# Optimization experiments

Hardware: AMD Instinct MI355X
Metric: run time of the kernel (lower is better)

## Reference

```python
import jax, jax.numpy as jnp
import numpy as np

D_MODEL = 192; D_STATE = 16; D_CONV = 4; D_INNER = 384; DT_RANK = 12; DEPTH = 8
B = 1; T = 8; IMG = 224; P = 16; GT = 8; GH = 14; GW = 14; L = 1 + GT * GH * GW
LN_EPS = 1e-5


def _layernorm(x, g, b):
    m = jnp.mean(x, -1, keepdims=True)
    v = jnp.var(x, -1, keepdims=True)
    return (x - m) * jax.lax.rsqrt(v + LN_EPS) * g + b


def _silu(x):
    return x * jax.nn.sigmoid(x)


def _mamba(h, W_in, Wc, bc, Wx, W_dt, b_dt, A_log, Dp, W_out):
    # h: (B, L, d_model)
    xz = h @ W_in.T                      # (B, L, 2*d_inner)
    u, z = jnp.split(xz, 2, axis=-1)
    Lh = h.shape[1]
    # causal depthwise conv1d (kernel D_CONV, left pad)
    up = jnp.pad(u, ((0, 0), (D_CONV - 1, 0), (0, 0)))
    uc = bc + sum(up[:, k:k + Lh, :] * Wc[:, k] for k in range(D_CONV))
    u = _silu(uc)
    xdbl = u @ Wx.T                      # (B, L, dt_rank + 2*d_state)
    dlt = xdbl[..., :DT_RANK]
    Bp = xdbl[..., DT_RANK:DT_RANK + D_STATE]
    Cp = xdbl[..., DT_RANK + D_STATE:]
    delta = jax.nn.softplus(dlt @ W_dt.T + b_dt)   # (B, L, d_inner)
    A = -jnp.exp(A_log)                  # (d_inner, d_state)
    dA = jnp.exp(delta[..., None] * A)                         # (B, L, Di, N)
    dBu = delta[..., None] * Bp[:, :, None, :] * u[..., None]  # (B, L, Di, N)

    def step(state, xs):
        dA_t, dBu_t, C_t = xs
        state = dA_t * state + dBu_t
        return state, jnp.einsum('bdn,bn->bd', state, C_t)

    s0 = jnp.zeros((h.shape[0], D_INNER, D_STATE), h.dtype)
    _, ys = jax.lax.scan(step, s0, (dA.transpose(1, 0, 2, 3), dBu.transpose(1, 0, 2, 3), Cp.transpose(1, 0, 2)))
    y = ys.transpose(1, 0, 2) + u * Dp
    y = y * _silu(z)
    return y @ W_out.T


def _forward(x, patch_w, patch_b, cls_tok, pos_emb, ln_g, ln_b, W_in, Wc, bc, Wx, W_dt, b_dt, A_log, Dp, W_out, fn_g, fn_b):
    b = x.shape[0]
    # tubelet patch embed: Conv3d kernel=stride=(1,16,16) as reshape+einsum
    xr = x.reshape(b, 3, GT, GH, P, GW, P)
    tok = jnp.einsum('bcthpwq,ecpq->bthwe', xr, patch_w) + patch_b
    tok = tok.reshape(b, GT * GH * GW, D_MODEL)
    tok = jnp.concatenate([jnp.broadcast_to(cls_tok, (b, 1, D_MODEL)), tok], axis=1) + pos_emb

    def block(c, p):
        g, bb, W_in_, Wc_, bc_, Wx_, W_dt_, b_dt_, A_log_, Dp_, W_out_ = p
        h = _layernorm(c, g, bb)
        return c + _mamba(h, W_in_, Wc_, bc_, Wx_, W_dt_, b_dt_, A_log_, Dp_, W_out_), None

    tok, _ = jax.lax.scan(block, tok, (ln_g, ln_b, W_in, Wc, bc, Wx, W_dt, b_dt, A_log, Dp, W_out))
    return _layernorm(tok, fn_g, fn_b)


def setup_inputs() -> dict:
    key = jax.random.key(0)
    ks = iter(jax.random.split(key, 64))

    def rn(shape, s=0.02):
        return jax.random.normal(next(ks), shape, jnp.float32) * s

    x = jax.random.normal(next(ks), (B, 3, T, IMG, IMG), jnp.float32)
    patch_w = rn((D_MODEL, 3, P, P))
    patch_b = jnp.zeros((D_MODEL,), jnp.float32)
    cls_tok = rn((1, 1, D_MODEL))
    pos_emb = rn((1, L, D_MODEL))
    ln_g = jnp.ones((DEPTH, D_MODEL), jnp.float32)
    ln_b = jnp.zeros((DEPTH, D_MODEL), jnp.float32)
    W_in = rn((DEPTH, 2 * D_INNER, D_MODEL))
    Wc = rn((DEPTH, D_INNER, D_CONV), 0.1)
    bc = jnp.zeros((DEPTH, D_INNER), jnp.float32)
    Wx = rn((DEPTH, DT_RANK + 2 * D_STATE, D_INNER))
    W_dt = rn((DEPTH, D_INNER, DT_RANK), DT_RANK ** -0.5)
    b_dt = jnp.zeros((DEPTH, D_INNER), jnp.float32)
    A_log = jnp.tile(jnp.log(jnp.arange(1, D_STATE + 1, dtype=jnp.float32)), (DEPTH, D_INNER, 1))
    Dp = jnp.ones((DEPTH, D_INNER), jnp.float32)
    W_out = rn((DEPTH, D_MODEL, D_INNER))
    fn_g = jnp.ones((D_MODEL,), jnp.float32)
    fn_b = jnp.zeros((D_MODEL,), jnp.float32)
    return dict(x=x, patch_w=patch_w, patch_b=patch_b, cls_tok=cls_tok, pos_emb=pos_emb,
                ln_g=ln_g, ln_b=ln_b, W_in=W_in, Wc=Wc, bc=bc, Wx=Wx, W_dt=W_dt, b_dt=b_dt,
                A_log=A_log, Dp=Dp, W_out=W_out, fn_g=fn_g, fn_b=fn_b)


def reference(x, patch_w, patch_b, cls_tok, pos_emb, ln_g, ln_b, W_in, Wc, bc, Wx, W_dt, b_dt, A_log, Dp, W_out, fn_g, fn_b):
    return _forward(x, patch_w, patch_b, cls_tok, pos_emb, ln_g, ln_b, W_in, Wc, bc, Wx, W_dt, b_dt, A_log, Dp, W_out, fn_g, fn_b)
```

## Files before the change

### kernel.cpp

```cpp
#include <hip/hip_runtime.h>
#include <hip/hip_bf16.h>
#include <math.h>

#define L_TOK 1569
#define DM 192
#define DI 384
#define DS 16
#define DTR 12
#define DCONV 4
#define XDBL_N (DTR + 2*DS)
#define DEPTH 8
#define NCHUNK 50
#define CLEN 32
#define NPATCH 1568
#define NDG 24

typedef __attribute__((ext_vector_type(8))) short short8;
typedef __attribute__((ext_vector_type(4))) float f32x4;

__device__ __forceinline__ unsigned short f2bf(float f) {
  unsigned int u = __float_as_uint(f);
  u += 0x7FFFu + ((u >> 16) & 1u);
  return (unsigned short)(u >> 16);
}

__global__ __launch_bounds__(256) void init_kernel(
    const float* __restrict__ cls, const float* __restrict__ pb,
    const float* __restrict__ pos, float* __restrict__ curp) {
  int gid = blockIdx.x * 256 + threadIdx.x;
  const int initN = (L_TOK * DM) / 4;
  if (gid >= initN) return;
  int e4 = gid * 4;
  int tok = e4 / DM;
  int col = e4 % DM;
  float4 pv = *(const float4*)(pos + e4);
  float4 av = (tok == 0) ? *(const float4*)(cls + col)
                         : *(const float4*)(pb + col);
  float4 o = {pv.x + av.x, pv.y + av.y, pv.z + av.z, pv.w + av.w};
  *(float4*)(curp + e4) = o;
}

__global__ __launch_bounds__(64) void ln_kernel(
    const float* __restrict__ in, float* __restrict__ out,
    const float* __restrict__ g, const float* __restrict__ b) {
  int tokn = blockIdx.x;
  int lane = threadIdx.x;
  const float* row = in + (size_t)tokn*DM;
  float x0 = row[lane], x1 = row[lane+64], x2 = row[lane+128];
  float s = x0 + x1 + x2;
  float s2 = x0*x0 + x1*x1 + x2*x2;
#pragma unroll
  for (int off = 1; off < 64; off <<= 1) {
    s  += __shfl_xor(s,  off, 64);
    s2 += __shfl_xor(s2, off, 64);
  }
  float m = s * (1.0f/192.0f);
  float v = s2 * (1.0f/192.0f) - m*m;
  float rs = rsqrtf(v + 1e-5f);
  float* orow = out + (size_t)tokn*DM;
  orow[lane]     = (x0 - m)*rs*g[lane]     + b[lane];
  orow[lane+64]  = (x1 - m)*rs*g[lane+64]  + b[lane+64];
  orow[lane+128] = (x2 - m)*rs*g[lane+128] + b[lane+128];
}

__device__ __forceinline__ float4 ldx4(const float* __restrict__ x,
                                       int pt, int hh, int w, int k) {
  int c = k >> 8, p = (k >> 4) & 15, q = k & 15;
  return *(const float4*)(x + ((size_t)(c*8 + pt)*224 + hh*16 + p)*224
                            + w*16 + q);
}

__global__ __launch_bounds__(256) void patch_gemm(
    const float* __restrict__ x, const float* __restrict__ pw,
    float* __restrict__ C) {
  __shared__ unsigned short As[64*40];
  __shared__ unsigned short Bs[64*40];
  int tid = threadIdx.x;
  int m0 = blockIdx.y * 64, n0 = blockIdx.x * 64;
  int kbase = blockIdx.z * 192;
  int wave = tid >> 6, lane = tid & 63;
  int wr = wave >> 1, wc = wave & 1;
  int srow = tid >> 2;
  int skq  = (tid & 3) * 8;
  f32x4 acc[2][2];
#pragma unroll
  for (int i = 0; i < 2; ++i)
#pragma unroll
    for (int j = 0; j < 2; ++j) acc[i][j] = (f32x4){0.f,0.f,0.f,0.f};

  int am = m0 + srow;
  bool a_ok = (am < NPATCH);
  int am_s = a_ok ? am : 0;
  int pt = am_s / 196, hw = am_s % 196, hh = hw / 14, w = hw % 14;
  int bn = n0 + srow;
  const float* bp = pw + (size_t)bn*768 + kbase + skq;
  const float4 z4 = {0.f,0.f,0.f,0.f};
  int l15 = lane & 15, lk = (lane >> 4) * 8;

  const int nt = 6;
  float4 a0 = a_ok ? ldx4(x, pt, hh, w, kbase + skq)     : z4;
  float4 a1 = a_ok ? ldx4(x, pt, hh, w, kbase + skq + 4) : z4;
  float4 b0 = *(const float4*)(bp);
  float4 b1 = *(const float4*)(bp + 4);

  for (int i = 0; i < nt; ++i) {
    {
      short8 pa, pb;
      pa[0]=f2bf(a0.x); pa[1]=f2bf(a0.y); pa[2]=f2bf(a0.z); pa[3]=f2bf(a0.w);
      pa[4]=f2bf(a1.x); pa[5]=f2bf(a1.y); pa[6]=f2bf(a1.z); pa[7]=f2bf(a1.w);
      pb[0]=f2bf(b0.x); pb[1]=f2bf(b0.y); pb[2]=f2bf(b0.z); pb[3]=f2bf(b0.w);
      pb[4]=f2bf(b1.x); pb[5]=f2bf(b1.y); pb[6]=f2bf(b1.z); pb[7]=f2bf(b1.w);
      *(short8*)&As[srow*40 + skq] = pa;
      *(short8*)&Bs[srow*40 + skq] = pb;
    }
    __syncthreads();
    bool pf = (i + 1 < nt);
    int kn = kbase + ((i + 1) << 5) + skq;
    a0 = (pf && a_ok) ? ldx4(x, pt, hh, w, kn)     : z4;
    a1 = (pf && a_ok) ? ldx4(x, pt, hh, w, kn + 4) : z4;
    b0 = pf ? *(const float4*)(bp + ((i+1)<<5))     : z4;
    b1 = pf ? *(const float4*)(bp + ((i+1)<<5) + 4) : z4;

    short8 af0 = *(const short8*)&As[(wr*32      + l15)*40 + lk];
    short8 af1 = *(const short8*)&As[(wr*32 + 16 + l15)*40 + lk];
    short8 bf0 = *(const short8*)&Bs[(wc*32      + l15)*40 + lk];
    short8 bf1 = *(const short8*)&Bs[(wc*32 + 16 + l15)*40 + lk];
    acc[0][0] = __builtin_amdgcn_mfma_f32_16x16x32_bf16(af0, bf0, acc[0][0], 0, 0, 0);
    acc[0][1] = __builtin_amdgcn_mfma_f32_16x16x32_bf16(af0, bf1, acc[0][1], 0, 0, 0);
    acc[1][0] = __builtin_amdgcn_mfma_f32_16x16x32_bf16(af1, bf0, acc[1][0], 0, 0, 0);
    acc[1][1] = __builtin_amdgcn_mfma_f32_16x16x32_bf16(af1, bf1, acc[1][1], 0, 0, 0);
    __syncthreads();
  }

#pragma unroll
  for (int r = 0; r < 2; ++r) {
#pragma unroll
    for (int c = 0; c < 2; ++c) {
      int col = n0 + wc*32 + c*16 + l15;
      int rowb = m0 + wr*32 + r*16 + (lane >> 4)*4;
#pragma unroll
      for (int j = 0; j < 4; ++j) {
        int row = rowb + j;
        if (row < NPATCH)
          atomicAdd(C + (size_t)row*DM + col, acc[r][c][j]);
      }
    }
  }
}

__global__ __launch_bounds__(256) void lnxz_kernel(
    const float* __restrict__ cur, const float* __restrict__ g,
    const float* __restrict__ b, const float* __restrict__ W,
    float* __restrict__ xz, float* __restrict__ xdbl_z) {
  __shared__ unsigned short As[64][200];
  __shared__ unsigned short Bs[64][200];
  __shared__ float gs[192], bs2[192];
  int tid = threadIdx.x;
  int m0 = blockIdx.y * 64, n0 = blockIdx.x * 64;
  int wave = tid >> 6, lane = tid & 63;
  int wr = wave >> 1, wc = wave & 1;
  int l15 = lane & 15, lk = (lane >> 4) * 8;

  for (int i = tid; i < 192; i += 256) { gs[i] = g[i]; bs2[i] = b[i]; }

  if (blockIdx.x == 0) {
    for (int i = tid; i < 64*11; i += 256) {
      int r = i / 11, q = i % 11;
      int row = m0 + r;
      if (row < L_TOK) {
        float4 z = {0.f,0.f,0.f,0.f};
        *(float4*)(xdbl_z + (size_t)row*XDBL_N + q*4) = z;
      }
    }
  }

  int r = tid >> 2, c0 = (tid & 3) * 48;
  float v[48];
  {
    int row = m0 + r;
    if (row < L_TOK) {
      const float* rp = cur + (size_t)row*DM + c0;
#pragma unroll
      for (int j = 0; j < 12; ++j) {
        float4 t4 = *(const float4*)(rp + j*4);
        v[j*4+0]=t4.x; v[j*4+1]=t4.y; v[j*4+2]=t4.z; v[j*4+3]=t4.w;
      }
    } else {
#pragma unroll
      for (int j = 0; j < 48; ++j) v[j] = 0.f;
    }
  }
  float s = 0.f, s2 = 0.f;
#pragma unroll
  for (int j = 0; j < 48; ++j) { s += v[j]; s2 += v[j]*v[j]; }
  s  += __shfl_xor(s, 1, 64); s2 += __shfl_xor(s2, 1, 64);
  s  += __shfl_xor(s, 2, 64); s2 += __shfl_xor(s2, 2, 64);
  float mu = s * (1.0f/192.0f);
  float var = s2 * (1.0f/192.0f) - mu*mu;
  float rsd = rsqrtf(var + 1e-5f);

  __syncthreads();
#pragma unroll
  for (int j = 0; j < 48; ++j) {
    int k = c0 + j;
    As[r][k] = f2bf((v[j] - mu)*rsd*gs[k] + bs2[k]);
  }
  {
    const float* rp = W + (size_t)(n0 + r)*DM + c0;
#pragma unroll
    for (int j = 0; j < 12; ++j) {
      float4 t4 = *(const float4*)(rp + j*4);
      Bs[r][c0+j*4+0]=f2bf(t4.x); Bs[r][c0+j*4+1]=f2bf(t4.y);
      Bs[r][c0+j*4+2]=f2bf(t4.z); Bs[r][c0+j*4+3]=f2bf(t4.w);
    }
  }
  __syncthreads();

  f32x4 acc[2][2];
#pragma unroll
  for (int i = 0; i < 2; ++i)
#pragma unroll
    for (int j = 0; j < 2; ++j) acc[i][j] = (f32x4){0.f,0.f,0.f,0.f};

#pragma unroll
  for (int kk = 0; kk < 6; ++kk) {
    short8 af0 = *(const short8*)&As[wr*32      + l15][kk*32 + lk];
    short8 af1 = *(const short8*)&As[wr*32 + 16 + l15][kk*32 + lk];
    short8 bf0 = *(const short8*)&Bs[wc*32      + l15][kk*32 + lk];
    short8 bf1 = *(const short8*)&Bs[wc*32 + 16 + l15][kk*32 + lk];
    acc[0][0] = __builtin_amdgcn_mfma_f32_16x16x32_bf16(af0, bf0, acc[0][0], 0, 0, 0);
    acc[0][1] = __builtin_amdgcn_mfma_f32_16x16x32_bf16(af0, bf1, acc[0][1], 0, 0, 0);
    acc[1][0] = __builtin_amdgcn_mfma_f32_16x16x32_bf16(af1, bf0, acc[1][0], 0, 0, 0);
    acc[1][1] = __builtin_amdgcn_mfma_f32_16x16x32_bf16(af1, bf1, acc[1][1], 0, 0, 0);
  }

#pragma unroll
  for (int rr = 0; rr < 2; ++rr) {
#pragma unroll
    for (int cc = 0; cc < 2; ++cc) {
      int col = n0 + wc*32 + cc*16 + l15;
      int rowb = m0 + wr*32 + rr*16 + (lane >> 4)*4;
#pragma unroll
      for (int j = 0; j < 4; ++j) {
        int row = rowb + j;
        if (row < L_TOK) xz[(size_t)row*(2*DI) + col] = acc[rr][cc][j];
      }
    }
  }
}

__global__ __launch_bounds__(256) void cgemm_kernel(
    const float* __restrict__ xz,
    const float* __restrict__ Wc, const float* __restrict__ bc,
    const float* __restrict__ B, float* __restrict__ C,
    float* __restrict__ uc) {
  __shared__ unsigned short As[64*40];
  __shared__ unsigned short Bs[64*40];
  __shared__ float wcs[32][4];
  __shared__ float bcs[32];
  const int M = L_TOK, N = XDBL_N;
  int tid = threadIdx.x;
  int m0 = blockIdx.y * 64;
  int kbase = blockIdx.z * 32;
  int wave = tid >> 6, lane = tid & 63;
  int wr = wave >> 1, wcq = wave & 1;
  int srow = tid >> 2;
  int skq  = (tid & 3) * 8;
  if (tid < 32) {
    *(float4*)wcs[tid] = *(const float4*)(Wc + (size_t)(kbase + tid)*4);
    bcs[tid] = bc[kbase + tid];
  }

  int t = m0 + srow;
  bool a_ok = (t < M);
  bool b_ok = (srow < N);
  const float* bp = B + (size_t)srow*DI + kbase + skq;
  const float4 z4 = {0.f,0.f,0.f,0.f};
  int l15 = lane & 15, lk = (lane >> 4) * 8;
  int cg = kbase + skq;

  float tap[4][8];
#pragma unroll
  for (int j = 0; j < 4; ++j) {
    int ts = t - 3 + j;
    float4 v0 = z4, v1 = z4;
    if (a_ok && ts >= 0) {
      v0 = *(const float4*)(xz + (size_t)ts*(2*DI) + cg);
      v1 = *(const float4*)(xz + (size_t)ts*(2*DI) + cg + 4);
    }
    tap[j][0]=v0.x; tap[j][1]=v0.y; tap[j][2]=v0.z; tap[j][3]=v0.w;
    tap[j][4]=v1.x; tap[j][5]=v1.y; tap[j][6]=v1.z; tap[j][7]=v1.w;
  }
  float4 bv0 = b_ok ? *(const float4*)(bp)     : z4;
  float4 bv1 = b_ok ? *(const float4*)(bp + 4) : z4;
  __syncthreads();

  float uv[8];
  short8 pa, pb;
#pragma unroll
  for (int c = 0; c < 8; ++c) {
    float u = bcs[skq + c];
#pragma unroll
    for (int j = 0; j < 4; ++j) u = fmaf(tap[j][c], wcs[skq + c][j], u);
    u = u / (1.0f + expf(-u));
    uv[c] = u;
    pa[c] = (short)f2bf(u);
  }
  if (a_ok) {
    float4 o0 = {uv[0], uv[1], uv[2], uv[3]};
    float4 o1 = {uv[4], uv[5], uv[6], uv[7]};
    *(float4*)(uc + (size_t)t*DI + cg)     = o0;
    *(float4*)(uc + (size_t)t*DI + cg + 4) = o1;
  }
  pb[0]=f2bf(bv0.x); pb[1]=f2bf(bv0.y); pb[2]=f2bf(bv0.z); pb[3]=f2bf(bv0.w);
  pb[4]=f2bf(bv1.x); pb[5]=f2bf(bv1.y); pb[6]=f2bf(bv1.z); pb[7]=f2bf(bv1.w);
  *(short8*)&As[srow*40 + skq] = pa;
  *(short8*)&Bs[srow*40 + skq] = pb;
  __syncthreads();

  f32x4 acc[2][2];
#pragma unroll
  for (int i = 0; i < 2; ++i)
#pragma unroll
    for (int j = 0; j < 2; ++j) acc[i][j] = (f32x4){0.f,0.f,0.f,0.f};
  short8 af0 = *(const short8*)&As[(wr*32      + l15)*40 + lk];
  short8 af1 = *(const short8*)&As[(wr*32 + 16 + l15)*40 + lk];
  short8 bf0 = *(const short8*)&Bs[(wcq*32      + l15)*40 + lk];
  short8 bf1 = *(const short8*)&Bs[(wcq*32 + 16 + l15)*40 + lk];
  acc[0][0] = __builtin_amdgcn_mfma_f32_16x16x32_bf16(af0, bf0, acc[0][0], 0, 0, 0);
  acc[0][1] = __builtin_amdgcn_mfma_f32_16x16x32_bf16(af0, bf1, acc[0][1], 0, 0, 0);
  acc[1][0] = __builtin_amdgcn_mfma_f32_16x16x32_bf16(af1, bf0, acc[1][0], 0, 0, 0);
  acc[1][1] = __builtin_amdgcn_mfma_f32_16x16x32_bf16(af1, bf1, acc[1][1], 0, 0, 0);

#pragma unroll
  for (int r = 0; r < 2; ++r) {
#pragma unroll
    for (int c = 0; c < 2; ++c) {
      int col = wcq*32 + c*16 + l15;
      if (col >= N) continue;
      int rowb = m0 + wr*32 + r*16 + (lane >> 4)*4;
#pragma unroll
      for (int j = 0; j < 4; ++j) {
        int row = rowb + j;
        if (row >= M) continue;
        atomicAdd(C + (size_t)row*XDBL_N + col, acc[r][c][j]);
      }
    }
  }
}

__global__ __launch_bounds__(256) void scan_p1(
    const float* __restrict__ uc, const float* __restrict__ xdbl,
    const float* __restrict__ W_dt, const float* __restrict__ b_dt,
    const float* __restrict__ A_log,
    float* __restrict__ cP, float* __restrict__ cS,
    float* __restrict__ dlt) {
  __shared__ float us[CLEN][16], ds[CLEN][16], bs[CLEN][16];
  __shared__ float xd12[CLEN][12], wdt[16][12], bds[16];
  int tid = threadIdx.x;
  int dl = tid >> 4, n = tid & 15;
  int d0 = blockIdx.x * 16;
  int t0 = blockIdx.y * CLEN;

  for (int i = tid; i < CLEN*16; i += 256) {
    int tt = i >> 4, dd = i & 15;
    int t = t0 + tt;
    us[tt][dd] = (t < L_TOK) ? uc[(size_t)t*DI + d0 + dd] : 0.0f;
  }
  for (int i = tid; i < CLEN*28; i += 256) {
    int tt = i / 28, c = i % 28;
    int t = t0 + tt;
    float v = (t < L_TOK) ? xdbl[(size_t)t*XDBL_N + c] : 0.0f;
    if (c < 12) xd12[tt][c] = v;
    else bs[tt][c-12] = v;
  }
  if (tid < 192) wdt[tid/12][tid%12] = W_dt[(d0 + tid/12)*DTR + tid%12];
  if (tid < 16)  bds[tid] = b_dt[d0+tid];
  __syncthreads();
  for (int i = tid; i < CLEN*16; i += 256) {
    int tt = i >> 4, dd = i & 15;
    int t = t0 + tt;
    float v = 0.0f;
    if (t < L_TOK) {
      v = bds[dd];
#pragma unroll
      for (int r = 0; r < 12; ++r) v = fmaf(xd12[tt][r], wdt[dd][r], v);
      v = (v > 20.0f) ? v : log1pf(expf(v));
      dlt[(size_t)t*DI + d0 + dd] = v;
    }
    ds[tt][dd] = v;
  }
  __syncthreads();

  int d = d0 + dl;
  float a2 = -expf(A_log[d*DS + n]) * 1.44269504088896340736f;
  float s = 0.0f, P = 1.0f;
#pragma unroll 4
  for (int tt = 0; tt < CLEN; ++tt) {
    float dv = ds[tt][dl];
    float dA = exp2f(dv * a2);
    s = fmaf(dA, s, dv * bs[tt][n] * us[tt][dl]);
    P *= dA;
  }
  int o = (blockIdx.y * DI + d) * DS + n;
  cP[o] = P;
  cS[o] = s;
}

__global__ __launch_bounds__(256) void scan_p3(
    const float* __restrict__ uc, const float* __restrict__ dlt,
    const float* __restrict__ xdbl, const float* __restrict__ xz,
    const float* __restrict__ A_log, const float* __restrict__ Dp,
    const float* __restrict__ cP, const float* __restrict__ cS,
    float* __restrict__ yy) {
  __shared__ float us[CLEN][16], ds[CLEN][16], bs[CLEN][16];
  __shared__ float cs[CLEN][16], zs[CLEN][16];
  int tid = threadIdx.x;
  int dl = tid >> 4, n = tid & 15;
  int d0 = blockIdx.x * 16;
  int cidx = blockIdx.y;
  int t0 = cidx * CLEN;
  int nt = min(CLEN, L_TOK - t0);
  int d = d0 + dl;

  float s = 0.0f;
  {
    int oo = d * DS + n;
    for (int c2 = 0; c2 < cidx; ++c2)
      s = fmaf(cP[(size_t)c2*(DI*DS) + oo], s, cS[(size_t)c2*(DI*DS) + oo]);
  }

  for (int i = tid; i < CLEN*16; i += 256) {
    int tt = i >> 4, dd = i & 15;
    int t = t0 + tt;
    bool ok = (t < L_TOK);
    us[tt][dd] = ok ? uc[(size_t)t*DI + d0 + dd] : 0.f;
    ds[tt][dd] = ok ? dlt[(size_t)t*DI + d0 + dd] : 0.f;
    zs[tt][dd] = ok ? xz[(size_t)t*(2*DI) + DI + d0 + dd] : 0.f;
  }
  for (int i = tid; i < CLEN*32; i += 256) {
    int tt = i >> 5, cq = i & 31;
    int t = t0 + tt;
    float v = (t < L_TOK) ? xdbl[(size_t)t*XDBL_N + 12 + cq] : 0.f;
    if (cq < 16) bs[tt][cq] = v;
    else cs[tt][cq-16] = v;
  }
  __syncthreads();

  float a2 = -expf(A_log[d*DS + n]) * 1.44269504088896340736f;
  float dpv = Dp[d];
#pragma unroll 4
  for (int tt = 0; tt < CLEN; ++tt) {
    float dv = ds[tt][dl], uu = us[tt][dl];
    float dA = exp2f(dv * a2);
    s = fmaf(dA, s, dv * bs[tt][n] * uu);
    float p = s * cs[tt][n];
    p += __shfl_xor(p, 1, 64);
    p += __shfl_xor(p, 2, 64);
    p += __shfl_xor(p, 4, 64);
    p += __shfl_xor(p, 8, 64);
    if (n == 0 && tt < nt) {
      float z = zs[tt][dl];
      float y = fmaf(uu, dpv, p);
      y *= z / (1.0f + expf(-z));
      yy[(size_t)(t0 + tt)*DI + d] = y;
    }
  }
}

__global__ __launch_bounds__(256) void mgemm_kernel(
    const float* __restrict__ A, int lda,
    const float* __restrict__ B, int ldb,
    float* __restrict__ C, int ldc,
    int M, int N, int ksl) {
  __shared__ unsigned short As[64*40];
  __shared__ unsigned short Bs[64*40];
  int tid = threadIdx.x;
  int m0 = blockIdx.y * 64, n0 = blockIdx.x * 64;
  int kbase = blockIdx.z * ksl;
  int wave = tid >> 6, lane = tid & 63;
  int wr = wave >> 1, wc = wave & 1;
  int srow = tid >> 2;
  int skq  = (tid & 3) * 8;
  f32x4 acc[2][2];
#pragma unroll
  for (int i = 0; i < 2; ++i)
#pragma unroll
    for (int j = 0; j < 2; ++j) acc[i][j] = (f32x4){0.f,0.f,0.f,0.f};

  int am = m0 + srow;
  int bn = n0 + srow;
  bool a_ok = (am < M), b_ok = (bn < N);
  const float* ap = A + (size_t)am*lda + kbase + skq;
  const float* bp = B + (size_t)bn*ldb + kbase + skq;
  const float4 z4 = {0.f,0.f,0.f,0.f};
  int l15 = lane & 15, lk = (lane >> 4) * 8;

  int nt = ksl >> 5;
  float4 a0 = a_ok ? *(const float4*)(ap)     : z4;
  float4 a1 = a_ok ? *(const float4*)(ap + 4) : z4;
  float4 b0 = b_ok ? *(const float4*)(bp)     : z4;
  float4 b1 = b_ok ? *(const float4*)(bp + 4) : z4;

  for (int i = 0; i < nt; ++i) {
    {
      short8 pa, pb;
      pa[0]=f2bf(a0.x); pa[1]=f2bf(a0.y); pa[2]=f2bf(a0.z); pa[3]=f2bf(a0.w);
      pa[4]=f2bf(a1.x); pa[5]=f2bf(a1.y); pa[6]=f2bf(a1.z); pa[7]=f2bf(a1.w);
      pb[0]=f2bf(b0.x); pb[1]=f2bf(b0.y); pb[2]=f2bf(b0.z); pb[3]=f2bf(b0.w);
      pb[4]=f2bf(b1.x); pb[5]=f2bf(b1.y); pb[6]=f2bf(b1.z); pb[7]=f2bf(b1.w);
      *(short8*)&As[srow*40 + skq] = pa;
      *(short8*)&Bs[srow*40 + skq] = pb;
    }
    __syncthreads();
    bool pf = (i + 1 < nt);
    int k0n = (i + 1) << 5;
    a0 = (pf && a_ok) ? *(const float4*)(ap + k0n)     : z4;
    a1 = (pf && a_ok) ? *(const float4*)(ap + k0n + 4) : z4;
    b0 = (pf && b_ok) ? *(const float4*)(bp + k0n)     : z4;
    b1 = (pf && b_ok) ? *(const float4*)(bp + k0n + 4) : z4;

    short8 af0 = *(const short8*)&As[(wr*32      + l15)*40 + lk];
    short8 af1 = *(const short8*)&As[(wr*32 + 16 + l15)*40 + lk];
    short8 bf0 = *(const short8*)&Bs[(wc*32      + l15)*40 + lk];
    short8 bf1 = *(const short8*)&Bs[(wc*32 + 16 + l15)*40 + lk];
    acc[0][0] = __builtin_amdgcn_mfma_f32_16x16x32_bf16(af0, bf0, acc[0][0], 0, 0, 0);
    acc[0][1] = __builtin_amdgcn_mfma_f32_16x16x32_bf16(af0, bf1, acc[0][1], 0, 0, 0);
    acc[1][0] = __builtin_amdgcn_mfma_f32_16x16x32_bf16(af1, bf0, acc[1][0], 0, 0, 0);
    acc[1][1] = __builtin_amdgcn_mfma_f32_16x16x32_bf16(af1, bf1, acc[1][1], 0, 0, 0);
    __syncthreads();
  }

#pragma unroll
  for (int r = 0; r < 2; ++r) {
#pragma unroll
    for (int c = 0; c < 2; ++c) {
      int col = n0 + wc*32 + c*16 + l15;
      if (col >= N) continue;
      int rowb = m0 + wr*32 + r*16 + (lane >> 4)*4;
#pragma unroll
      for (int j = 0; j < 4; ++j) {
        int row = rowb + j;
        if (row >= M) continue;
        atomicAdd(C + (size_t)row*ldc + col, acc[r][c][j]);
      }
    }
  }
}

extern "C" void kernel_launch(void* const* d_in, const int* in_sizes, int n_in,
                              void* d_out, int out_size, void* d_ws, size_t ws_size,
                              hipStream_t stream) {
  const float* x       = (const float*)d_in[0];
  const float* patch_w = (const float*)d_in[1];
  const float* patch_b = (const float*)d_in[2];
  const float* cls_tok = (const float*)d_in[3];
  const float* pos_emb = (const float*)d_in[4];
  const float* ln_g    = (const float*)d_in[5];
  const float* ln_b    = (const float*)d_in[6];
  const float* W_in    = (const float*)d_in[7];
  const float* Wc      = (const float*)d_in[8];
  const float* bc      = (const float*)d_in[9];
  const float* Wx      = (const float*)d_in[10];
  const float* W_dt    = (const float*)d_in[11];
  const float* b_dt    = (const float*)d_in[12];
  const float* A_log   = (const float*)d_in[13];
  const float* Dp      = (const float*)d_in[14];
  const float* W_out   = (const float*)d_in[15];
  const float* fn_g    = (const float*)d_in[16];
  const float* fn_b    = (const float*)d_in[17];

  float* ws = (float*)d_ws;
  float* cur   = ws;
  float* xz    = cur   + L_TOK*DM;
  float* xdbl  = xz    + L_TOK*2*DI;
  float* uc    = xdbl  + L_TOK*XDBL_N;
  float* dlt   = uc    + L_TOK*DI;
  float* yy    = dlt   + L_TOK*DI;
  float* cP    = yy    + L_TOK*DI;
  float* cS    = cP    + NCHUNK*DI*DS;

  init_kernel<<<(L_TOK*DM/4 + 255)/256, 256, 0, stream>>>(
      cls_tok, patch_b, pos_emb, cur);
  {
    dim3 grid(DM/64, (NPATCH + 63)/64, 4);
    patch_gemm<<<grid, 256, 0, stream>>>(x, patch_w, cur + DM);
  }

  for (int dep = 0; dep < DEPTH; ++dep) {
    const float* g     = ln_g  + dep*DM;
    const float* bb    = ln_b  + dep*DM;
    const float* Win_l = W_in  + (size_t)dep*2*DI*DM;
    const float* Wc_l  = Wc    + (size_t)dep*DI*DCONV;
    const float* bc_l  = bc    + (size_t)dep*DI;
    const float* Wx_l  = Wx    + (size_t)dep*XDBL_N*DI;
    const float* Wdt_l = W_dt  + (size_t)dep*DI*DTR;
    const float* bdt_l = b_dt  + (size_t)dep*DI;
    const float* Alog_l= A_log + (size_t)dep*DI*DS;
    const float* Dp_l  = Dp    + (size_t)dep*DI;
    const float* Wout_l= W_out + (size_t)dep*DM*DI;

    {
      dim3 grid((2*DI)/64, (L_TOK + 63)/64);
      lnxz_kernel<<<grid, 256, 0, stream>>>(cur, g, bb, Win_l, xz, xdbl);
    }
    {
      dim3 grid(1, (L_TOK + 63)/64, 12);
      cgemm_kernel<<<grid, 256, 0, stream>>>(xz, Wc_l, bc_l, Wx_l, xdbl, uc);
    }
    {
      dim3 g1(NDG, NCHUNK);
      scan_p1<<<g1, 256, 0, stream>>>(uc, xdbl, Wdt_l, bdt_l, Alog_l, cP, cS, dlt);
      scan_p3<<<g1, 256, 0, stream>>>(uc, dlt, xdbl, xz, Alog_l, Dp_l, cP, cS, yy);
    }
    {
      dim3 grid(DM/64, (L_TOK + 63)/64, 4);
      mgemm_kernel<<<grid, 256, 0, stream>>>(yy, DI, Wout_l, DI, cur, DM,
                                             L_TOK, DM, DI/4);
    }
  }

  ln_kernel<<<L_TOK, 64, 0, stream>>>(cur, (float*)d_out, fn_g, fn_b);
}
```

Before: 586.9 us.

## Store intermediate activations xz, uc, delta, y in bf16 instead of fp32

Intermediate activation buffers passed between kernels (xz, the conv/silu output, delta and the gated scan output) are now stored as bf16 rather than fp32, and every producer and consumer kernel is changed to match. This halves the global memory traffic for these tensors and lets the output GEMM stage its A operand directly without converting. The scan also uses the bf16-rounded delta so that both passes see identical values. The cost is extra rounding error in the z gate, u and delta values fed to the recurrence, which could move results against the fp32 reference.

```diff
diff --git a/kernel.cpp b/kernel.cpp
--- a/kernel.cpp
+++ b/kernel.cpp
@@ -16,12 +16,17 @@
 #define NDG 24
 
 typedef __attribute__((ext_vector_type(8))) short short8;
+typedef __attribute__((ext_vector_type(8))) unsigned short us8;
 typedef __attribute__((ext_vector_type(4))) float f32x4;
 
 __device__ __forceinline__ unsigned short f2bf(float f) {
   unsigned int u = __float_as_uint(f);
   u += 0x7FFFu + ((u >> 16) & 1u);
   return (unsigned short)(u >> 16);
+}
+
+__device__ __forceinline__ float bf2f(unsigned short h) {
+  return __uint_as_float(((unsigned int)h) << 16);
 }
 
 __global__ __launch_bounds__(256) void init_kernel(
@@ -151,7 +156,7 @@
 __global__ __launch_bounds__(256) void lnxz_kernel(
     const float* __restrict__ cur, const float* __restrict__ g,
     const float* __restrict__ b, const float* __restrict__ W,
-    float* __restrict__ xz, float* __restrict__ xdbl_z) {
+    unsigned short* __restrict__ xzb, float* __restrict__ xdbl_z) {
   __shared__ unsigned short As[64][200];
   __shared__ unsigned short Bs[64][200];
   __shared__ float gs[192], bs2[192];
@@ -243,17 +248,18 @@
 #pragma unroll
       for (int j = 0; j < 4; ++j) {
         int row = rowb + j;
-        if (row < L_TOK) xz[(size_t)row*(2*DI) + col] = acc[rr][cc][j];
+        if (row < L_TOK)
+          xzb[(size_t)row*(2*DI) + col] = f2bf(acc[rr][cc][j]);
       }
     }
   }
 }
 
 __global__ __launch_bounds__(256) void cgemm_kernel(
-    const float* __restrict__ xz,
+    const unsigned short* __restrict__ xzb,
     const float* __restrict__ Wc, const float* __restrict__ bc,
     const float* __restrict__ B, float* __restrict__ C,
-    float* __restrict__ uc) {
+    unsigned short* __restrict__ ucb) {
   __shared__ unsigned short As[64*40];
   __shared__ unsigned short Bs[64*40];
   __shared__ float wcs[32][4];
@@ -276,42 +282,33 @@
   bool b_ok = (srow < N);
   const float* bp = B + (size_t)srow*DI + kbase + skq;
   const float4 z4 = {0.f,0.f,0.f,0.f};
+  const us8 z8 = {0,0,0,0,0,0,0,0};
   int l15 = lane & 15, lk = (lane >> 4) * 8;
   int cg = kbase + skq;
 
-  float tap[4][8];
+  us8 tap[4];
 #pragma unroll
   for (int j = 0; j < 4; ++j) {
     int ts = t - 3 + j;
-    float4 v0 = z4, v1 = z4;
-    if (a_ok && ts >= 0) {
-      v0 = *(const float4*)(xz + (size_t)ts*(2*DI) + cg);
-      v1 = *(const float4*)(xz + (size_t)ts*(2*DI) + cg + 4);
-    }
-    tap[j][0]=v0.x; tap[j][1]=v0.y; tap[j][2]=v0.z; tap[j][3]=v0.w;
-    tap[j][4]=v1.x; tap[j][5]=v1.y; tap[j][6]=v1.z; tap[j][7]=v1.w;
+    tap[j] = (a_ok && ts >= 0)
+               ? *(const us8*)(xzb + (size_t)ts*(2*DI) + cg) : z8;
   }
   float4 bv0 = b_ok ? *(const float4*)(bp)     : z4;
   float4 bv1 = b_ok ? *(const float4*)(bp + 4) : z4;
   __syncthreads();
 
-  float uv[8];
   short8 pa, pb;
 #pragma unroll
   for (int c = 0; c < 8; ++c) {
     float u = bcs[skq + c];
 #pragma unroll
-    for (int j = 0; j < 4; ++j) u = fmaf(tap[j][c], wcs[skq + c][j], u);
+    for (int j = 0; j < 4; ++j)
+      u = fmaf(bf2f(tap[j][c]), wcs[skq + c][j], u);
     u = u / (1.0f + expf(-u));
-    uv[c] = u;
     pa[c] = (short)f2bf(u);
   }
-  if (a_ok) {
-    float4 o0 = {uv[0], uv[1], uv[2], uv[3]};
-    float4 o1 = {uv[4], uv[5], uv[6], uv[7]};
-    *(float4*)(uc + (size_t)t*DI + cg)     = o0;
-    *(float4*)(uc + (size_t)t*DI + cg + 4) = o1;
-  }
+  if (a_ok)
+    *(short8*)(ucb + (size_t)t*DI + cg) = pa;
   pb[0]=f2bf(bv0.x); pb[1]=f2bf(bv0.y); pb[2]=f2bf(bv0.z); pb[3]=f2bf(bv0.w);
   pb[4]=f2bf(bv1.x); pb[5]=f2bf(bv1.y); pb[6]=f2bf(bv1.z); pb[7]=f2bf(bv1.w);
   *(short8*)&As[srow*40 + skq] = pa;
@@ -350,22 +347,25 @@
 }
 
 __global__ __launch_bounds__(256) void scan_p1(
-    const float* __restrict__ uc, const float* __restrict__ xdbl,
+    const unsigned short* __restrict__ ucb, const float* __restrict__ xdbl,
     const float* __restrict__ W_dt, const float* __restrict__ b_dt,
     const float* __restrict__ A_log,
     float* __restrict__ cP, float* __restrict__ cS,
-    float* __restrict__ dlt) {
+    unsigned short* __restrict__ dltb) {
   __shared__ float us[CLEN][16], ds[CLEN][16], bs[CLEN][16];
   __shared__ float xd12[CLEN][12], wdt[16][12], bds[16];
   int tid = threadIdx.x;
   int dl = tid >> 4, n = tid & 15;
   int d0 = blockIdx.x * 16;
   int t0 = blockIdx.y * CLEN;
-
-  for (int i = tid; i < CLEN*16; i += 256) {
-    int tt = i >> 4, dd = i & 15;
+  const us8 z8 = {0,0,0,0,0,0,0,0};
+
+  for (int i = tid; i < CLEN*2; i += 256) {
+    int tt = i >> 1, h = (i & 1) * 8;
     int t = t0 + tt;
-    us[tt][dd] = (t < L_TOK) ? uc[(size_t)t*DI + d0 + dd] : 0.0f;
+    us8 v = (t < L_TOK) ? *(const us8*)(ucb + (size_t)t*DI + d0 + h) : z8;
+#pragma unroll
+    for (int j = 0; j < 8; ++j) us[tt][h+j] = bf2f(v[j]);
   }
   for (int i = tid; i < CLEN*28; i += 256) {
     int tt = i / 28, c = i % 28;
@@ -386,7 +386,9 @@
 #pragma unroll
       for (int r = 0; r < 12; ++r) v = fmaf(xd12[tt][r], wdt[dd][r], v);
       v = (v > 20.0f) ? v : log1pf(expf(v));
-      dlt[(size_t)t*DI + d0 + dd] = v;
+      unsigned short hb = f2bf(v);
+      dltb[(size_t)t*DI + d0 + dd] = hb;
+      v = bf2f(hb);
     }
     ds[tt][dd] = v;
   }
@@ -408,11 +410,12 @@
 }
 
 __global__ __launch_bounds__(256) void scan_p3(
-    const float* __restrict__ uc, const float* __restrict__ dlt,
-    const float* __restrict__ xdbl, const float* __restrict__ xz,
+    const unsigned short* __restrict__ ucb,
+    const unsigned short* __restrict__ dltb,
+    const float* __restrict__ xdbl, const unsigned short* __restrict__ xzb,
     const float* __restrict__ A_log, const float* __restrict__ Dp,
     const float* __restrict__ cP, const float* __restrict__ cS,
-    float* __restrict__ yy) {
+    unsigned short* __restrict__ yyb) {
   __shared__ float us[CLEN][16], ds[CLEN][16], bs[CLEN][16];
   __shared__ float cs[CLEN][16], zs[CLEN][16];
   int tid = threadIdx.x;
@@ -422,6 +425,7 @@
   int t0 = cidx * CLEN;
   int nt = min(CLEN, L_TOK - t0);
   int d = d0 + dl;
+  const us8 z8 = {0,0,0,0,0,0,0,0};
 
   float s = 0.0f;
   {
@@ -430,13 +434,19 @@
       s = fmaf(cP[(size_t)c2*(DI*DS) + oo], s, cS[(size_t)c2*(DI*DS) + oo]);
   }
 
-  for (int i = tid; i < CLEN*16; i += 256) {
-    int tt = i >> 4, dd = i & 15;
+  for (int i = tid; i < CLEN*2; i += 256) {
+    int tt = i >> 1, h = (i & 1) * 8;
     int t = t0 + tt;
     bool ok = (t < L_TOK);
-    us[tt][dd] = ok ? uc[(size_t)t*DI + d0 + dd] : 0.f;
-    ds[tt][dd] = ok ? dlt[(size_t)t*DI + d0 + dd] : 0.f;
-    zs[tt][dd] = ok ? xz[(size_t)t*(2*DI) + DI + d0 + dd] : 0.f;
+    us8 vu = ok ? *(const us8*)(ucb  + (size_t)t*DI + d0 + h) : z8;
+    us8 vd = ok ? *(const us8*)(dltb + (size_t)t*DI + d0 + h) : z8;
+    us8 vz = ok ? *(const us8*)(xzb  + (size_t)t*(2*DI) + DI + d0 + h) : z8;
+#pragma unroll
+    for (int j = 0; j < 8; ++j) {
+      us[tt][h+j] = bf2f(vu[j]);
+      ds[tt][h+j] = bf2f(vd[j]);
+      zs[tt][h+j] = bf2f(vz[j]);
+    }
   }
   for (int i = tid; i < CLEN*32; i += 256) {
     int tt = i >> 5, cq = i & 31;
@@ -463,13 +473,13 @@
       float z = zs[tt][dl];
       float y = fmaf(uu, dpv, p);
       y *= z / (1.0f + expf(-z));
-      yy[(size_t)(t0 + tt)*DI + d] = y;
+      yyb[(size_t)(t0 + tt)*DI + d] = f2bf(y);
     }
   }
 }
 
 __global__ __launch_bounds__(256) void mgemm_kernel(
-    const float* __restrict__ A, int lda,
+    const unsigned short* __restrict__ A, int lda,
     const float* __restrict__ B, int ldb,
     float* __restrict__ C, int ldc,
     int M, int N, int ksl) {
@@ -491,32 +501,29 @@
   int am = m0 + srow;
   int bn = n0 + srow;
   bool a_ok = (am < M), b_ok = (bn < N);
-  const float* ap = A + (size_t)am*lda + kbase + skq;
+  const unsigned short* ap = A + (size_t)am*lda + kbase + skq;
   const float* bp = B + (size_t)bn*ldb + kbase + skq;
   const float4 z4 = {0.f,0.f,0.f,0.f};
+  const us8 z8 = {0,0,0,0,0,0,0,0};
   int l15 = lane & 15, lk = (lane >> 4) * 8;
 
   int nt = ksl >> 5;
-  float4 a0 = a_ok ? *(const float4*)(ap)     : z4;
-  float4 a1 = a_ok ? *(const float4*)(ap + 4) : z4;
+  us8 av = a_ok ? *(const us8*)(ap) : z8;
   float4 b0 = b_ok ? *(const float4*)(bp)     : z4;
   float4 b1 = b_ok ? *(const float4*)(bp + 4) : z4;
 
   for (int i = 0; i < nt; ++i) {
     {
-      short8 pa, pb;
-      pa[0]=f2bf(a0.x); pa[1]=f2bf(a0.y); pa[2]=f2bf(a0.z); pa[3]=f2bf(a0.w);
-      pa[4]=f2bf(a1.x); pa[5]=f2bf(a1.y); pa[6]=f2bf(a1.z); pa[7]=f2bf(a1.w);
+      short8 pb;
       pb[0]=f2bf(b0.x); pb[1]=f2bf(b0.y); pb[2]=f2bf(b0.z); pb[3]=f2bf(b0.w);
       pb[4]=f2bf(b1.x); pb[5]=f2bf(b1.y); pb[6]=f2bf(b1.z); pb[7]=f2bf(b1.w);
-      *(short8*)&As[srow*40 + skq] = pa;
+      *(us8*)&As[srow*40 + skq] = av;
       *(short8*)&Bs[srow*40 + skq] = pb;
     }
     __syncthreads();
     bool pf = (i + 1 < nt);
     int k0n = (i + 1) << 5;
-    a0 = (pf && a_ok) ? *(const float4*)(ap + k0n)     : z4;
-    a1 = (pf && a_ok) ? *(const float4*)(ap + k0n + 4) : z4;
+    av = (pf && a_ok) ? *(const us8*)(ap + k0n) : z8;
     b0 = (pf && b_ok) ? *(const float4*)(bp + k0n)     : z4;
     b1 = (pf && b_ok) ? *(const float4*)(bp + k0n + 4) : z4;
 
@@ -572,13 +579,13 @@
 
   float* ws = (float*)d_ws;
   float* cur   = ws;
-  float* xz    = cur   + L_TOK*DM;
-  float* xdbl  = xz    + L_TOK*2*DI;
-  float* uc    = xdbl  + L_TOK*XDBL_N;
-  float* dlt   = uc    + L_TOK*DI;
-  float* yy    = dlt   + L_TOK*DI;
-  float* cP    = yy    + L_TOK*DI;
-  float* cS    = cP    + NCHUNK*DI*DS;
+  unsigned short* xzb = (unsigned short*)(cur + L_TOK*DM);
+  float* xdbl  = (float*)(xzb + L_TOK*2*DI);
+  unsigned short* ucb  = (unsigned short*)(xdbl + L_TOK*XDBL_N);
+  unsigned short* dltb = ucb  + L_TOK*DI;
+  unsigned short* yyb  = dltb + L_TOK*DI;
+  float* cP    = (float*)(yyb + L_TOK*DI);
+  float* cS    = cP + NCHUNK*DI*DS;
 
   init_kernel<<<(L_TOK*DM/4 + 255)/256, 256, 0, stream>>>(
       cls_tok, patch_b, pos_emb, cur);
@@ -602,20 +609,20 @@
 
     {
       dim3 grid((2*DI)/64, (L_TOK + 63)/64);
-      lnxz_kernel<<<grid, 256, 0, stream>>>(cur, g, bb, Win_l, xz, xdbl);
+      lnxz_kernel<<<grid, 256, 0, stream>>>(cur, g, bb, Win_l, xzb, xdbl);
     }
     {
       dim3 grid(1, (L_TOK + 63)/64, 12);
-      cgemm_kernel<<<grid, 256, 0, stream>>>(xz, Wc_l, bc_l, Wx_l, xdbl, uc);
+      cgemm_kernel<<<grid, 256, 0, stream>>>(xzb, Wc_l, bc_l, Wx_l, xdbl, ucb);
     }
     {
       dim3 g1(NDG, NCHUNK);
-      scan_p1<<<g1, 256, 0, stream>>>(uc, xdbl, Wdt_l, bdt_l, Alog_l, cP, cS, dlt);
-      scan_p3<<<g1, 256, 0, stream>>>(uc, dlt, xdbl, xz, Alog_l, Dp_l, cP, cS, yy);
+      scan_p1<<<g1, 256, 0, stream>>>(ucb, xdbl, Wdt_l, bdt_l, Alog_l, cP, cS, dltb);
+      scan_p3<<<g1, 256, 0, stream>>>(ucb, dltb, xdbl, xzb, Alog_l, Dp_l, cP, cS, yyb);
     }
     {
       dim3 grid(DM/64, (L_TOK + 63)/64, 4);
-      mgemm_kernel<<<grid, 256, 0, stream>>>(yy, DI, Wout_l, DI, cur, DM,
+      mgemm_kernel<<<grid, 256, 0, stream>>>(yyb, DI, Wout_l, DI, cur, DM,
                                              L_TOK, DM, DI/4);
     }
   }
```

Measured after the change: 542.8 us. -7.5%, faster.
